# Kernel optimization log

Measured on AMD Instinct MI355X. Metric: run time of the kernel, lower is better.

## Reference

```python
import jax, jax.numpy as jnp
import numpy as np

N = 729        # problem variables
B = 8          # batch
K = 32         # mixing rank (hard-coded in MixingFunc)
NB = 40        # number of symmetry-basis matrices
MAX_ITER = 10  # coordinate-descent sweeps


def setup_inputs() -> dict:
    key = jax.random.key(0)
    ks = jax.random.split(key, 7)
    coeff = jax.random.normal(ks[0], (NB,), jnp.float32)
    upper = jax.random.normal(ks[1], (N,), jnp.float32)
    basis = jax.random.normal(ks[2], (NB, N, N), jnp.float32)
    z = jax.random.uniform(ks[3], (B, N), jnp.float32)
    is_input = jax.random.randint(ks[4], (B, N), 0, 2).astype(jnp.int32)
    v_init_raw = jax.random.normal(ks[5], (B, N + 1, K), jnp.float32)
    # random permutation of the N non-truth variables (indices 1..N), as in satnet init
    perm = (jax.random.permutation(ks[6], N) + 1).astype(jnp.int32)
    return dict(coeff=coeff, upper=upper, basis=basis, z=z,
                is_input=is_input, v_init_raw=v_init_raw, perm=perm)


def _build_C(coeff, upper, basis):
    # BasisFunc.forward: C = [[0, upper^T], [upper, sum_b coeff_b * basis_b]]
    center = jnp.einsum('b,bij->ij', coeff, basis)              # (N, N)
    top = jnp.concatenate([jnp.zeros((1,), upper.dtype), upper])[None, :]  # (1, N+1)
    bottom = jnp.concatenate([upper[:, None], center], axis=1)  # (N, N+1)
    return jnp.concatenate([top, bottom], axis=0)               # (N+1, N+1)


def _init_V(v_raw, z_full):
    # SATNet init: v0 = random unit truth direction; each v_i is placed on the
    # cone around v0 at angle pi*z_i using a random orthogonal direction.
    v0 = v_raw[:, 0] / jnp.linalg.norm(v_raw[:, 0], axis=-1, keepdims=True)  # (B, K)
    dot = jnp.einsum('bnk,bk->bn', v_raw, v0)
    u = v_raw - dot[..., None] * v0[:, None, :]
    u = u / jnp.maximum(jnp.linalg.norm(u, axis=-1, keepdims=True), 1e-8)
    c = jnp.cos(jnp.pi * z_full)[..., None]
    s = jnp.sin(jnp.pi * z_full)[..., None]
    V = -c * v0[:, None, :] + s * u                              # (B, N+1, K)
    V = V.at[:, 0].set(v0)                                       # truth vector pinned
    return V


def _mix(C, V, is_input_full, perm):
    # SATNet mixing coordinate descent: for each free variable i,
    #   g_i = sum_j C[j,i] v_j - C[i,i] v_i ;  v_i <- -g_i / ||g_i||
    Cdiag = jnp.diagonal(C)
    free = (is_input_full == 0)                                  # (B, N+1)

    def coord_step(V, i):
        g = jnp.einsum('j,bjk->bk', C[:, i], V) - Cdiag[i] * V[:, i]  # (B, K)
        gn = jnp.linalg.norm(g, axis=-1, keepdims=True)
        vnew = -g / jnp.maximum(gn, 1e-8)
        V = V.at[:, i].set(jnp.where(free[:, i][:, None], vnew, V[:, i]))
        return V, None

    def sweep(V, _):
        V, _ = jax.lax.scan(coord_step, V, perm)
        return V, None

    V, _ = jax.lax.scan(jax.checkpoint(sweep), V, None, length=MAX_ITER)
    return V


def reference(coeff, upper, basis, z, is_input, v_init_raw, perm):
    Bn = z.shape[0]
    C = _build_C(coeff, upper, basis)
    z_full = jnp.concatenate([jnp.ones((Bn, 1), z.dtype), z], axis=1)
    ii_full = jnp.concatenate(
        [jnp.ones((Bn, 1), is_input.dtype), is_input], axis=1)
    V = _init_V(v_init_raw, z_full)
    V = _mix(C, V, ii_full, perm)
    v0 = V[:, 0]
    cosang = jnp.clip(-jnp.einsum('bnk,bk->bn', V, v0), -1.0 + 1e-6, 1.0 - 1e-6)
    zo = jnp.arccos(cosang) / jnp.pi
    z_out = jnp.where(ii_full == 1, z_full, zo)
    return z_out[:, 1:]
```

## Files before the change

kernel.cpp:

```cpp
#include <hip/hip_runtime.h>

#define NN   729
#define NF   730
#define BV   8
#define KK   32
#define NBAS 40
#define MAXIT 10
#define PI_F 3.14159265358979323846f

#define MTH   512
#define BT    16
#define AST   448

typedef float v2f __attribute__((ext_vector_type(2)));

__device__ __forceinline__ void fma4(float4& w, float c, const float4& d) {
    w.x = fmaf(c, d.x, w.x); w.y = fmaf(c, d.y, w.y);
    w.z = fmaf(c, d.z, w.z); w.w = fmaf(c, d.w, w.w);
}

__global__ void build_C_kernel(const float* __restrict__ coeff,
                               const float* __restrict__ upper,
                               const float* __restrict__ basis,
                               float* __restrict__ Ct) {
    int idx = blockIdx.x * blockDim.x + threadIdx.x;
    if (idx >= NF * NF) return;
    int i = idx / NF, j = idx - i * NF;
    float val;
    if (i == 0) {
        val = (j == 0) ? 0.f : upper[j - 1];
    } else if (j == 0) {
        val = upper[i - 1];
    } else {
        float acc = 0.f;
        const float* bp = basis + (size_t)(i - 1) * NN + (j - 1);
        #pragma unroll 8
        for (int b = 0; b < NBAS; ++b)
            acc = fmaf(coeff[b], bp[(size_t)b * NN * NN], acc);
        val = acc;
    }
    Ct[(size_t)j * NF + i] = val;
}

__global__ void init_V_kernel(const float* __restrict__ z,
                              const float* __restrict__ vraw,
                              float* __restrict__ V) {
    int g = threadIdx.x >> 5;
    int k = threadIdx.x & 31;
    int row = blockIdx.x * 8 + g;
    int b = row / NF, n = row - b * NF;
    const float* vr = vraw + (size_t)b * NF * KK;

    float v0 = vr[k];
    float s2 = v0 * v0;
    #pragma unroll
    for (int off = 16; off; off >>= 1) s2 += __shfl_xor(s2, off, 32);
    v0 = v0 / sqrtf(s2);

    float vn = vr[(size_t)n * KK + k];
    float d = vn * v0;
    #pragma unroll
    for (int off = 16; off; off >>= 1) d += __shfl_xor(d, off, 32);
    float u = vn - d * v0;
    float un2 = u * u;
    #pragma unroll
    for (int off = 16; off; off >>= 1) un2 += __shfl_xor(un2, off, 32);
    u = u / fmaxf(sqrtf(un2), 1e-8f);

    float zf = (n == 0) ? 1.f : z[b * NN + (n - 1)];
    float c = cosf(PI_F * zf), s = sinf(PI_F * zf);
    float outv = -c * v0 + s * u;
    if (n == 0) outv = v0;
    V[((size_t)b * NF + n) * KK + k] = outv;
}

__global__ void build_act_kernel(const int* __restrict__ is_input,
                                 const int* __restrict__ perm,
                                 int* __restrict__ act, int* __restrict__ nA_arr) {
    int b = blockIdx.x, l = threadIdx.x;
    int base = 0;
    for (int c = 0; c < (NN + 63) / 64; ++c) {
        int idx = c * 64 + l;
        bool f = false; int pi = 0;
        if (idx < NN) { pi = perm[idx]; f = (is_input[b * NN + pi - 1] == 0); }
        unsigned long long m = __ballot(f);
        int pos = __popcll(m & ((1ull << l) - 1ull));
        if (f && base + pos < AST) act[b * AST + base + pos] = pi;
        base += __popcll(m);
    }
    if (base > AST) base = AST;
    if (l == 0) nA_arr[b] = base;
    for (int p = base + l; p < AST; p += 64) act[b * AST + p] = 0;
}

__global__ void gather_CactT_kernel(const float* __restrict__ Ct,
                                    const int* __restrict__ act,
                                    float* __restrict__ CactT) {
    int a = blockIdx.x, b = blockIdx.y;
    __shared__ int acts[AST];
    for (int i = threadIdx.x; i < AST; i += blockDim.x) acts[i] = act[b * AST + i];
    __syncthreads();
    const float* src = Ct + (size_t)acts[a] * NF;
    float* dst = CactT + ((size_t)b * AST + a) * AST;
    for (int t = threadIdx.x; t < AST; t += blockDim.x)
        dst[t] = src[acts[t]];
}

__global__ void init_W_kernel(const float* __restrict__ Ct,
                              const int* __restrict__ act,
                              const int* __restrict__ nA_arr,
                              const float* __restrict__ V,
                              float* __restrict__ Wc,
                              float* __restrict__ Vact) {
    int b = blockIdx.y;
    int a = blockIdx.x * 8 + (threadIdx.x >> 5);
    int k = threadIdx.x & 31;
    int nA = nA_arr[b];
    float w = 0.f;
    int ra = act[b * AST + a];
    float vv = V[((size_t)b * NF + ra) * KK + k];
    if (a < nA) {
        const float* ctr = Ct + (size_t)ra * NF;
        const float* vb = V + (size_t)b * NF * KK + k;
        float acc = 0.f;
        for (int j = 0; j < NF; ++j)
            acc = fmaf(ctr[j], vb[(size_t)j * KK], acc);
        w = acc - ctr[ra] * vv;
    }
    Wc[((size_t)b * AST + a) * KK + k] = w;
    Vact[((size_t)b * AST + a) * KK + k] = vv;
}

__device__ __forceinline__ float rowsum16(float x) {
    int y;
    y = __builtin_amdgcn_update_dpp(0, __float_as_int(x), 0x121, 0xF, 0xF, false);
    x += __int_as_float(y);
    y = __builtin_amdgcn_update_dpp(0, __float_as_int(x), 0x122, 0xF, 0xF, false);
    x += __int_as_float(y);
    y = __builtin_amdgcn_update_dpp(0, __float_as_int(x), 0x124, 0xF, 0xF, false);
    x += __int_as_float(y);
    y = __builtin_amdgcn_update_dpp(0, __float_as_int(x), 0x128, 0xF, 0xF, false);
    x += __int_as_float(y);
    return x;
}

__global__ __launch_bounds__(MTH, 2)
void mix_kernel(const float* __restrict__ CactT_g,
                const float* __restrict__ Wc_g,
                const float* __restrict__ Vact_g,
                const int* __restrict__ act_g,
                const int* __restrict__ nA_arr,
                const int* __restrict__ is_input,
                const float* __restrict__ z,
                const float* __restrict__ Vg,
                float* __restrict__ out) {
    __shared__ __align__(16) float V_c[AST * KK];
    __shared__ __align__(16) float dv_s[2][BT * KK];
    __shared__ __align__(16) float gpub[2][BT * KK];
    __shared__ __align__(16) float cblk_s[2][BT * BT];
    __shared__ __align__(16) float cminiT_s[2][BT * BT];
    __shared__ float Cd_s[AST];
    __shared__ int   slot_s[NF];

    int b = blockIdx.x, tid = threadIdx.x;
    const float* CT = CactT_g + (size_t)b * AST * AST;
    const float* Vact = Vact_g + (size_t)b * AST * KK;
    int nA = nA_arr[b];
    int nblkp = (nA + BT - 1) / BT;
    if (nblkp < 2) nblkp = 2;
    int nAp = nblkp * BT;
    int totB = MAXIT * nblkp;

    int wid = tid >> 6;
    int l64 = tid & 63;
    int lane = tid - 64;
    int kq = lane & 7;
    int rslot = lane >> 3;
    int kp = tid & 15;

    for (int idx = tid; idx < AST * 8; idx += MTH)
        ((float4*)V_c)[idx] = ((const float4*)Vact)[idx];
    if (tid < AST) Cd_s[tid] = CT[(size_t)tid * AST + tid];
    if (tid < nA) slot_s[act_g[b * AST + tid]] = tid;
    if (tid < 256) {
        int t = tid >> 4, u = tid & 15;
        cblk_s[0][t * BT + u] = CT[(size_t)u * AST + t];
    }
    float4 w[8];
    #pragma unroll
    for (int p = 0; p < 8; ++p) {
        float4 zz = {0.f, 0.f, 0.f, 0.f};
        w[p] = zz;
        if (wid >= 1)
            w[p] = *(const float4*)&Wc_g[((size_t)b * AST + rslot + 56 * p) * KK + 4 * kq];
    }
    if (wid >= 1) {
        #pragma unroll
        for (int p = 0; p < 8; ++p) {
            int a = rslot + 56 * p;
            if ((a >> 4) == 0)
                *(float4*)&gpub[1][a * KK + 4 * kq] = w[p];
        }
    }
    __syncthreads();

    for (int bi = 0; bi < totB; ++bi) {
        int blk = bi % nblkp, s0 = blk * BT;
        int pblk = (bi - 1 + nblkp) % nblkp, sp0 = pblk * BT;
        int cb = bi & 1, pv = cb ^ 1;
        int nblk2 = (bi + 1) % nblkp, sn0 = nblk2 * BT;

        if (wid == 0) {
            float g0[BT], g1[BT], vo0[BT], vo1[BT];
            #pragma unroll
            for (int u = 0; u < BT; ++u) {
                v2f gv = *(const v2f*)&gpub[pv][u * KK + 2 * kp];
                g0[u] = gv.x; g1[u] = gv.y;
                v2f vv = *(const v2f*)&V_c[(s0 + u) * KK + 2 * kp];
                vo0[u] = vv.x; vo1[u] = vv.y;
            }
            if (bi > 0) {
                #pragma unroll
                for (int t = 0; t < BT; ++t) {
                    v2f dp = *(const v2f*)&dv_s[pv][t * KK + 2 * kp];
                    #pragma unroll
                    for (int q = 0; q < 4; ++q) {
                        float4 cm = *(const float4*)&cminiT_s[cb][t * BT + 4 * q];
                        g0[4*q+0] = fmaf(cm.x, dp.x, g0[4*q+0]);
                        g1[4*q+0] = fmaf(cm.x, dp.y, g1[4*q+0]);
                        g0[4*q+1] = fmaf(cm.y, dp.x, g0[4*q+1]);
                        g1[4*q+1] = fmaf(cm.y, dp.y, g1[4*q+1]);
                        g0[4*q+2] = fmaf(cm.z, dp.x, g0[4*q+2]);
                        g1[4*q+2] = fmaf(cm.z, dp.y, g1[4*q+2]);
                        g0[4*q+3] = fmaf(cm.w, dp.x, g0[4*q+3]);
                        g1[4*q+3] = fmaf(cm.w, dp.y, g1[4*q+3]);
                    }
                }
            }
            #pragma unroll
            for (int u = 0; u < BT; ++u) {
                int s = s0 + u;
                float n2 = fmaf(g0[u], g0[u], g1[u] * g1[u]);
                n2 = rowsum16(n2);
                float inv = -__builtin_amdgcn_rsqf(fmaxf(n2, 1e-16f));
                float msk = (s < nA) ? 1.f : 0.f;
                float d0 = fmaf(g0[u], inv, -vo0[u]) * msk;
                float d1 = fmaf(g1[u], inv, -vo1[u]) * msk;
                if (tid < 16) {
                    v2f dv2; dv2.x = d0; dv2.y = d1;
                    *(v2f*)&dv_s[cb][u * KK + 2 * kp] = dv2;
                    v2f vn2; vn2.x = vo0[u] + d0; vn2.y = vo1[u] + d1;
                    *(v2f*)&V_c[s * KK + 2 * kp] = vn2;
                }
                #pragma unroll
                for (int u2 = u + 1; u2 < BT; ++u2) {
                    float c = cblk_s[cb][u * BT + u2];
                    g0[u2] = fmaf(c, d0, g0[u2]);
                    g1[u2] = fmaf(c, d1, g1[u2]);
                }
            }
        } else {
            if (wid == 6) {
                int u = l64 & 15, q = l64 >> 4;
                float4 v = *(const float4*)&CT[(size_t)(sn0 + u) * AST + s0 + 4 * q];
                cminiT_s[pv][(4 * q + 0) * BT + u] = v.x;
                cminiT_s[pv][(4 * q + 1) * BT + u] = v.y;
                cminiT_s[pv][(4 * q + 2) * BT + u] = v.z;
                cminiT_s[pv][(4 * q + 3) * BT + u] = v.w;
            }
            if (wid == 7) {
                int u = l64 & 15, q = l64 >> 4;
                float4 v = *(const float4*)&CT[(size_t)(sn0 + u) * AST + sn0 + 4 * q];
                cblk_s[pv][(4 * q + 0) * BT + u] = v.x;
                cblk_s[pv][(4 * q + 1) * BT + u] = v.y;
                cblk_s[pv][(4 * q + 2) * BT + u] = v.z;
                cblk_s[pv][(4 * q + 3) * BT + u] = v.w;
            }
            if (bi > 0) {
                #pragma unroll
                for (int h = 0; h < 2; ++h) {
                    float4 dvv[8];
                    #pragma unroll
                    for (int t = 0; t < 8; ++t)
                        dvv[t] = *(const float4*)&dv_s[pv][(8 * h + t) * KK + 4 * kq];
                    float4 cA0, cB0, cA1, cB1;
                    {
                        const float* cr = CT + (size_t)rslot * AST + sp0 + 8 * h;
                        cA0 = *(const float4*)(cr);
                        cB0 = *(const float4*)(cr + 4);
                    }
                    #pragma unroll
                    for (int p = 0; p < 8; ++p) {
                        int a = rslot + 56 * p;
                        if (p < 7) {
                            const float* cr = CT + (size_t)(a + 56) * AST + sp0 + 8 * h;
                            if (p & 1) { cA0 = *(const float4*)(cr); cB0 = *(const float4*)(cr + 4); }
                            else       { cA1 = *(const float4*)(cr); cB1 = *(const float4*)(cr + 4); }
                        }
                        float4 ca = (p & 1) ? cA1 : cA0;
                        float4 cbq = (p & 1) ? cB1 : cB0;
                        if (a < nAp) {
                            fma4(w[p], ca.x,  dvv[0]);
                            fma4(w[p], ca.y,  dvv[1]);
                            fma4(w[p], ca.z,  dvv[2]);
                            fma4(w[p], ca.w,  dvv[3]);
                            fma4(w[p], cbq.x, dvv[4]);
                            fma4(w[p], cbq.y, dvv[5]);
                            fma4(w[p], cbq.z, dvv[6]);
                            fma4(w[p], cbq.w, dvv[7]);
                        }
                    }
                }
                #pragma unroll
                for (int p = 0; p < 8; ++p) {
                    int a = rslot + 56 * p;
                    if ((a >> 4) == pblk) {
                        float4 dd = *(const float4*)&dv_s[pv][(a - sp0) * KK + 4 * kq];
                        fma4(w[p], -Cd_s[a], dd);
                    }
                }
            }
            #pragma unroll
            for (int p = 0; p < 8; ++p) {
                int a = rslot + 56 * p;
                if ((a >> 4) == nblk2)
                    *(float4*)&gpub[cb][(a - sn0) * KK + 4 * kq] = w[p];
            }
        }
        __syncthreads();
    }

    int k = tid & 31, r = tid >> 5;
    float v0k = Vg[(size_t)b * NF * KK + k];
    for (int n = 1 + r; n <= NN; n += 16) {
        int ii = is_input[b * NN + n - 1];
        float res;
        if (ii == 1) {
            res = z[b * NN + n - 1];
        } else {
            int a = slot_s[n];
            float dot = V_c[a * KK + k] * v0k;
            #pragma unroll
            for (int off = 16; off; off >>= 1) dot += __shfl_xor(dot, off, 32);
            float ca = fminf(fmaxf(-dot, -1.f + 1e-6f), 1.f - 1e-6f);
            res = acosf(ca) * (1.f / PI_F);
        }
        if (k == 0) out[b * NN + n - 1] = res;
    }
}

extern "C" void kernel_launch(void* const* d_in, const int* in_sizes, int n_in,
                              void* d_out, int out_size, void* d_ws, size_t ws_size,
                              hipStream_t stream) {
    const float* coeff    = (const float*)d_in[0];
    const float* upper    = (const float*)d_in[1];
    const float* basis    = (const float*)d_in[2];
    const float* z        = (const float*)d_in[3];
    const int*   is_input = (const int*)d_in[4];
    const float* vraw     = (const float*)d_in[5];
    const int*   perm     = (const int*)d_in[6];
    float* out = (float*)d_out;

    float* ws    = (float*)d_ws;
    float* Ct    = ws;
    float* V     = Ct + (size_t)NF * NF;
    float* CactT = V + (size_t)BV * NF * KK;
    float* Wc    = CactT + (size_t)BV * AST * AST;
    float* Vact  = Wc + (size_t)BV * AST * KK;
    int*   act   = (int*)(Vact + (size_t)BV * AST * KK);
    int*   nAa   = act + BV * AST;

    build_C_kernel<<<dim3((NF * NF + 255) / 256), dim3(256), 0, stream>>>(coeff, upper, basis, Ct);
    init_V_kernel<<<dim3(730), dim3(256), 0, stream>>>(z, vraw, V);
    build_act_kernel<<<dim3(BV), dim3(64), 0, stream>>>(is_input, perm, act, nAa);
    gather_CactT_kernel<<<dim3(AST, BV), dim3(256), 0, stream>>>(Ct, act, CactT);
    init_W_kernel<<<dim3(AST / 8, BV), dim3(256), 0, stream>>>(Ct, act, nAa, V, Wc, Vact);
    mix_kernel<<<dim3(BV), dim3(MTH), 0, stream>>>(CactT, Wc, Vact, act, nAa, is_input, z, V, out);
}
```

Measured before the change: 858.1 us.

## Move cross-block gradient correction off the serial warp into a block-wide pass

The serial wavefront 0 previously applied the previous block's update contribution (cmini times dv) to its gradients before the sequential coordinate updates. That correction is now done by all 512 threads in a separate phase after the main barrier, and the result is written back into gpub for the next iteration. The C mini-block is stored untransposed in a single buffer. This shortens the critical serial path, but it adds a second __syncthreads per block iteration, which may eat the gain.

```diff
diff --git a/kernel.cpp b/kernel.cpp
--- a/kernel.cpp
+++ b/kernel.cpp
@@ -158,7 +158,7 @@
     __shared__ __align__(16) float dv_s[2][BT * KK];
     __shared__ __align__(16) float gpub[2][BT * KK];
     __shared__ __align__(16) float cblk_s[2][BT * BT];
-    __shared__ __align__(16) float cminiT_s[2][BT * BT];
+    __shared__ __align__(16) float cmini_s[BT * BT];
     __shared__ float Cd_s[AST];
     __shared__ int   slot_s[NF];
 
@@ -218,24 +218,6 @@
                 g0[u] = gv.x; g1[u] = gv.y;
                 v2f vv = *(const v2f*)&V_c[(s0 + u) * KK + 2 * kp];
                 vo0[u] = vv.x; vo1[u] = vv.y;
-            }
-            if (bi > 0) {
-                #pragma unroll
-                for (int t = 0; t < BT; ++t) {
-                    v2f dp = *(const v2f*)&dv_s[pv][t * KK + 2 * kp];
-                    #pragma unroll
-                    for (int q = 0; q < 4; ++q) {
-                        float4 cm = *(const float4*)&cminiT_s[cb][t * BT + 4 * q];
-                        g0[4*q+0] = fmaf(cm.x, dp.x, g0[4*q+0]);
-                        g1[4*q+0] = fmaf(cm.x, dp.y, g1[4*q+0]);
-                        g0[4*q+1] = fmaf(cm.y, dp.x, g0[4*q+1]);
-                        g1[4*q+1] = fmaf(cm.y, dp.y, g1[4*q+1]);
-                        g0[4*q+2] = fmaf(cm.z, dp.x, g0[4*q+2]);
-                        g1[4*q+2] = fmaf(cm.z, dp.y, g1[4*q+2]);
-                        g0[4*q+3] = fmaf(cm.w, dp.x, g0[4*q+3]);
-                        g1[4*q+3] = fmaf(cm.w, dp.y, g1[4*q+3]);
-                    }
-                }
             }
             #pragma unroll
             for (int u = 0; u < BT; ++u) {
@@ -263,10 +245,7 @@
             if (wid == 6) {
                 int u = l64 & 15, q = l64 >> 4;
                 float4 v = *(const float4*)&CT[(size_t)(sn0 + u) * AST + s0 + 4 * q];
-                cminiT_s[pv][(4 * q + 0) * BT + u] = v.x;
-                cminiT_s[pv][(4 * q + 1) * BT + u] = v.y;
-                cminiT_s[pv][(4 * q + 2) * BT + u] = v.z;
-                cminiT_s[pv][(4 * q + 3) * BT + u] = v.w;
+                *(float4*)&cmini_s[u * BT + 4 * q] = v;
             }
             if (wid == 7) {
                 int u = l64 & 15, q = l64 >> 4;
@@ -328,6 +307,16 @@
             }
         }
         __syncthreads();
+
+        {
+            int u = tid >> 5, k = tid & 31;
+            float g = gpub[cb][u * KK + k];
+            #pragma unroll
+            for (int t = 0; t < BT; ++t)
+                g = fmaf(cmini_s[u * BT + t], dv_s[cb][t * KK + k], g);
+            gpub[cb][u * KK + k] = g;
+        }
+        __syncthreads();
     }
 
     int k = tid & 31, r = tid >> 5;
```

Result: faster. 743.6 us (-13.3%).
